# Kernel optimization log

Measured on AMD Instinct MI355X. Metric: run time of the kernel, lower is better.

The kernel has to match this reference:

```python
import jax, jax.numpy as jnp
import numpy as np

B, F, D = 1024, 64, 64  # batch, num fields, embedding dim


def setup_inputs() -> dict:
    key = jax.random.key(0)
    ks = jax.random.split(key, 7)
    return {
        "x": jax.random.normal(ks[0], (B, F, D), dtype=jnp.float32),
        "W1": jax.random.normal(ks[1], (F, F * F), dtype=jnp.float32) * 0.02,
        "b1": jax.random.normal(ks[2], (F,), dtype=jnp.float32) * 0.02,
        "W2": jax.random.normal(ks[3], (F, F * F), dtype=jnp.float32) * 0.02,
        "b2": jax.random.normal(ks[4], (F,), dtype=jnp.float32) * 0.02,
        "Wfc": jax.random.normal(ks[5], (1, 2 * F), dtype=jnp.float32) * 0.02,
        "bfc": jax.random.normal(ks[6], (1,), dtype=jnp.float32) * 0.02,
    }


def reference(x, W1, b1, W2, b2, Wfc, bfc):
    # x: [B, F, D]. CIN layer: outer product over field dims, 1x1 conv (channel
    # contraction with weight [F, F*F]), ReLU.
    b_, f0, d = x.shape
    x0 = x[:, :, None, :]  # [B, F, 1, D]
    h = x
    xs = []
    for W, b in ((W1, b1), (W2, b2)):
        z = (x0 * h[:, None, :, :]).reshape(b_, f0 * f0, d)  # [B, F*F, D]
        h = jax.nn.relu(jnp.einsum('oc,bcd->bod', W, z) + b[None, :, None])  # [B, F, D]
        xs.append(h)
    pooled = jnp.sum(jnp.concatenate(xs, axis=1), axis=2)  # [B, 2F] sum-pool over D
    return pooled @ Wfc.T + bfc  # [B, 1]
```

## Files before the change

### kernel.cpp

```cpp
#include <hip/hip_runtime.h>

typedef short s16x4 __attribute__((ext_vector_type(4)));
typedef short s16x8 __attribute__((ext_vector_type(8)));
typedef float f32x2 __attribute__((ext_vector_type(2)));
typedef float f32x16 __attribute__((ext_vector_type(16)));
typedef unsigned int u32x2 __attribute__((ext_vector_type(2)));
typedef unsigned int u32x4 __attribute__((ext_vector_type(4)));

#define HT_STRIDE 72

__device__ __forceinline__ unsigned short f2bf(float f) {
    unsigned int u = __float_as_uint(f);
    u += 0x7fffu + ((u >> 16) & 1u);
    return (unsigned short)(u >> 16);
}
__device__ __forceinline__ unsigned int pk2bf_rne(float lo, float hi) {
    unsigned int a = __float_as_uint(lo);
    a += 0x7fffu + ((a >> 16) & 1u);
    unsigned int b = __float_as_uint(hi);
    b += 0x7fffu + ((b >> 16) & 1u);
    return (a >> 16) | (b & 0xffff0000u);
}

__global__ __launch_bounds__(256) void prepack_kernel(const float* __restrict__ W1,
                                                      const float* __restrict__ W2,
                                                      unsigned short* __restrict__ Wp) {
    int tid = blockIdx.x * 256 + threadIdx.x;
    int lane = tid & 63;
    int ks = (tid >> 6) & 3;
    int jt = (tid >> 8) & 1;
    int o = (tid >> 9) & 63;
    int l = tid >> 15;
    int q2 = lane >> 5;
    int n31 = lane & 31;
    const float* W = l ? W2 : W1;
    const float* base = W + o * 4096 + jt * 32 + n31;
    int i0 = 16 * ks + 8 * q2;
    float v[8];
#pragma unroll
    for (int t = 0; t < 8; ++t) v[t] = base[(i0 + t) * 64];
    u32x4 pv;
    pv[0] = pk2bf_rne(v[0], v[1]);
    pv[1] = pk2bf_rne(v[2], v[3]);
    pv[2] = pk2bf_rne(v[4], v[5]);
    pv[3] = pk2bf_rne(v[6], v[7]);
    ((u32x4*)Wp)[tid] = pv;
}

__global__ __launch_bounds__(256, 2) void cin_kernel(const float* __restrict__ x,
                                                     const unsigned short* __restrict__ Wp,
                                                     const float* __restrict__ b1,
                                                     const float* __restrict__ b2,
                                                     const float* __restrict__ Wfc,
                                                     const float* __restrict__ bfc,
                                                     float* __restrict__ out) {
    __shared__ __align__(16) unsigned short sH[2][64 * HT_STRIDE];
    __shared__ float sBias[128], sWfc[128], sRed[4];

    const int tid = threadIdx.x;
    const int w = tid >> 6;
    const int lane = tid & 63;
    const int q2 = lane >> 5;
    const int n31 = lane & 31;
    const int oh = w;
    const int bb = blockIdx.x;

    {
        const float4* xb4 = (const float4*)(x + bb * 4096);
#pragma unroll
        for (int rr = 0; rr < 4; ++rr) {
            int e4 = rr * 256 + tid;
            float4 v = xb4[e4];
            int e = e4 << 2;
            int f = e >> 6;
            int d0 = e & 63;
            sH[0][(d0 + 0) * HT_STRIDE + f] = f2bf(v.x);
            sH[0][(d0 + 1) * HT_STRIDE + f] = f2bf(v.y);
            sH[0][(d0 + 2) * HT_STRIDE + f] = f2bf(v.z);
            sH[0][(d0 + 3) * HT_STRIDE + f] = f2bf(v.w);
        }
    }
    if (tid < 128) {
        sBias[tid] = (tid < 64) ? b1[tid] : b2[tid - 64];
        sWfc[tid] = Wfc[tid];
    }
    __syncthreads();

    const f32x16 zz = {};
    float contrib = 0.0f;
    const s16x8* WpS8 = (const s16x8*)Wp;

    s16x8 bfr[2][4];
#pragma unroll
    for (int nt = 0; nt < 2; ++nt) {
        const int d = nt * 32 + n31;
#pragma unroll
        for (int ks = 0; ks < 4; ++ks)
            bfr[nt][ks] = *(const s16x8*)&sH[0][d * HT_STRIDE + 16 * ks + 8 * q2];
    }

#define CONSUME(NT, ACC, JT, O)                                                   \
    {                                                                             \
        const f32x2* a2 = (const f32x2*)&(ACC);                                   \
        f32x2 s0 = {0.0f, 0.0f}, s1 = {0.0f, 0.0f};                               \
        _Pragma("unroll") for (int m = 0; m < 4; ++m) {                           \
            unsigned int qlo = cwp[NT][JT][m][0];                                 \
            unsigned int qhi = cwp[NT][JT][m][1];                                 \
            f32x2 c0 = {__uint_as_float(qlo << 16),                               \
                        __uint_as_float(qlo & 0xffff0000u)};                      \
            f32x2 c1 = {__uint_as_float(qhi << 16),                               \
                        __uint_as_float(qhi & 0xffff0000u)};                      \
            s0 += a2[2 * m] * c0;                                                 \
            s1 += a2[2 * m + 1] * c1;                                             \
        }                                                                         \
        f32x2 s = s0 + s1;                                                        \
        if ((JT) == 0) {                                                          \
            hp[NT] = s;                                                           \
        } else {                                                                  \
            f32x2 t2 = hp[NT] + s;                                                \
            float hsum = t2.x + t2.y;                                             \
            hsum += __shfl_xor(hsum, 32, 64);           \
            float v = fmaxf(hsum + sBias[l * 64 + (O)], 0.0f);                    \
            contrib += v * sWfc[l * 64 + (O)];                                    \
            if (l == 0)     \
                sH[1][((NT) * 32 + n31) * HT_STRIDE + (O)] = f2bf(v);             \
        }                                                                         \
    }

    for (int l = 0; l < 2; ++l) {
        if (l) __syncthreads();

        const unsigned short* hsrc = sH[l];
        u32x2 cwp[2][2][4];
#pragma unroll
        for (int nt = 0; nt < 2; ++nt) {
            const int d = nt * 32 + n31;
#pragma unroll
            for (int jt = 0; jt < 2; ++jt)
#pragma unroll
                for (int m = 0; m < 4; ++m)
                    cwp[nt][jt][m] =
                        *(const u32x2*)&hsrc[d * HT_STRIDE + jt * 32 + 4 * q2 + 8 * m];
        }

        s16x8 Areg[2][4];
        {
            const int F0 = (l * 128 + 2 * oh) * 4;
            const s16x8* p = WpS8 + F0 * 64 + lane;
#pragma unroll
            for (int ks = 0; ks < 4; ++ks) Areg[0][ks] = p[ks * 64];
        }
        f32x2 hp[2];

#pragma unroll 2
        for (int it = 0; it < 32; ++it) {
            const int jt = it & 1;
            const int o = 4 * (it >> 1) + oh;
            if (it < 31) {
                const int itn = it + 1;
                const int on = 4 * (itn >> 1) + oh;
                const int Fn = (l * 128 + 2 * on + (itn & 1)) * 4;
                const s16x8* p = WpS8 + Fn * 64 + lane;
#pragma unroll
                for (int ks = 0; ks < 4; ++ks) Areg[(it + 1) & 1][ks] = p[ks * 64];
            }
            const s16x8* A = Areg[it & 1];

            f32x16 a0 = __builtin_amdgcn_mfma_f32_32x32x16_bf16(A[0], bfr[0][0], zz, 0, 0, 0);
            a0 = __builtin_amdgcn_mfma_f32_32x32x16_bf16(A[1], bfr[0][1], a0, 0, 0, 0);
            a0 = __builtin_amdgcn_mfma_f32_32x32x16_bf16(A[2], bfr[0][2], a0, 0, 0, 0);
            a0 = __builtin_amdgcn_mfma_f32_32x32x16_bf16(A[3], bfr[0][3], a0, 0, 0, 0);
            CONSUME(0, a0, jt, o);
            __builtin_amdgcn_sched_barrier(0);

            f32x16 a1 = __builtin_amdgcn_mfma_f32_32x32x16_bf16(A[0], bfr[1][0], zz, 0, 0, 0);
            a1 = __builtin_amdgcn_mfma_f32_32x32x16_bf16(A[1], bfr[1][1], a1, 0, 0, 0);
            a1 = __builtin_amdgcn_mfma_f32_32x32x16_bf16(A[2], bfr[1][2], a1, 0, 0, 0);
            a1 = __builtin_amdgcn_mfma_f32_32x32x16_bf16(A[3], bfr[1][3], a1, 0, 0, 0);
            CONSUME(1, a1, jt, o);
        }
    }
#undef CONSUME

    contrib *= 0.5f;
#pragma unroll
    for (int off = 32; off > 0; off >>= 1)
        contrib += __shfl_down(contrib, off, 64);
    if (lane == 0) sRed[w] = contrib;
    __syncthreads();
    if (tid == 0)
        out[bb] = (sRed[0] + sRed[1]) + (sRed[2] + sRed[3]) + bfc[0];
}

extern "C" void kernel_launch(void* const* d_in, const int* in_sizes, int n_in,
                              void* d_out, int out_size, void* d_ws, size_t ws_size,
                              hipStream_t stream) {
    const float* x = (const float*)d_in[0];
    const float* W1 = (const float*)d_in[1];
    const float* b1 = (const float*)d_in[2];
    const float* W2 = (const float*)d_in[3];
    const float* b2 = (const float*)d_in[4];
    const float* Wfc = (const float*)d_in[5];
    const float* bfc = (const float*)d_in[6];
    float* out = (float*)d_out;

    unsigned short* Wp = (unsigned short*)d_ws;

    prepack_kernel<<<256, 256, 0, stream>>>(W1, W2, Wp);
    cin_kernel<<<1024, 256, 0, stream>>>(x, Wp, b1, b2, Wfc, bfc, out);
}
```

Baseline: 143.5 us.

## Deepen weight prefetch to a 4-stage inline-asm pipeline spanning both layers

Replaces the double-buffered weight-fragment loads with a 4-slot register ring filled by inline-asm global_load_dwordx4, issued three iterations ahead and continuing across the layer boundary. Explicit s_waitcnt vmcnt counts ensure only the current slot is complete before its MFMAs run. The two MFMA chains are also interleaved so both accumulators advance together instead of back to back. The aim is to hide global/L2 latency of the weight stream behind the matrix math, at the cost of more VGPRs, which could hurt occupancy with launch_bounds(256,2), and fragile hand-managed wait counts.

```diff
diff --git a/kernel.cpp b/kernel.cpp
--- a/kernel.cpp
+++ b/kernel.cpp
@@ -21,6 +21,10 @@
     b += 0x7fffu + ((b >> 16) & 1u);
     return (a >> 16) | (b & 0xffff0000u);
 }
+
+#define GLOADX4(dst, base, OFF)                                       \
+    asm volatile("global_load_dwordx4 %0, %1, off offset:" OFF        \
+                 : "=&v"(dst) : "v"(base) : "memory")
 
 __global__ __launch_bounds__(256) void prepack_kernel(const float* __restrict__ W1,
                                                       const float* __restrict__ W2,
@@ -64,6 +68,7 @@
     const int n31 = lane & 31;
     const int oh = w;
     const int bb = blockIdx.x;
+    const char* WpB = (const char*)Wp;
 
     {
         const float4* xb4 = (const float4*)(x + bb * 4096);
@@ -88,7 +93,19 @@
 
     const f32x16 zz = {};
     float contrib = 0.0f;
-    const s16x8* WpS8 = (const s16x8*)Wp;
+
+    s16x8 Ar[4][4];
+
+#pragma unroll
+    for (int g0 = 0; g0 < 3; ++g0) {
+        const int F = (8 * (g0 >> 1) + 2 * oh + (g0 & 1)) * 4;
+        const char* gp = WpB + (size_t)F * 1024 + lane * 16;
+        GLOADX4(Ar[g0][0], gp, "0");
+        GLOADX4(Ar[g0][1], gp, "1024");
+        GLOADX4(Ar[g0][2], gp, "2048");
+        GLOADX4(Ar[g0][3], gp, "3072");
+    }
+    __builtin_amdgcn_sched_barrier(0);
 
     s16x8 bfr[2][4];
 #pragma unroll
@@ -127,6 +144,44 @@
         }                                                                         \
     }
 
+#define ITER(IT, S)                                                               \
+    {                                                                             \
+        const int it_ = (IT);                                                     \
+        const int jt = it_ & 1;                                                   \
+        const int o = 4 * (it_ >> 1) + oh;                                        \
+        const int g = l * 32 + it_;                                               \
+        if (g < 61) {                                                             \
+            const int gn = g + 3;                                                 \
+            const int ln = gn >> 5, itn = gn & 31;                                \
+            const int Fn = (ln * 128 + 8 * (itn >> 1) + 2 * oh + (itn & 1)) * 4;  \
+            const char* gp = WpB + (size_t)Fn * 1024 + lane * 16;                 \
+            GLOADX4(Ar[((S) + 3) & 3][0], gp, "0");                               \
+            GLOADX4(Ar[((S) + 3) & 3][1], gp, "1024");                            \
+            GLOADX4(Ar[((S) + 3) & 3][2], gp, "2048");                            \
+            GLOADX4(Ar[((S) + 3) & 3][3], gp, "3072");                            \
+        }                                                                         \
+        __builtin_amdgcn_sched_barrier(0);                                        \
+        if (g < 61) {                                                             \
+            asm volatile("s_waitcnt vmcnt(12)" ::: "memory");                     \
+        } else if (g == 61) {                                                     \
+            asm volatile("s_waitcnt vmcnt(8)" ::: "memory");                      \
+        } else if (g == 62) {                                                     \
+            asm volatile("s_waitcnt vmcnt(4)" ::: "memory");                      \
+        } else {                                                                  \
+            asm volatile("s_waitcnt vmcnt(0)" ::: "memory");                      \
+        }                                                                         \
+        __builtin_amdgcn_sched_barrier(0);                                        \
+        const s16x8* A = Ar[(S)];                                                 \
+        f32x16 a0 = __builtin_amdgcn_mfma_f32_32x32x16_bf16(A[0], bfr[0][0], zz, 0, 0, 0); \
+        f32x16 a1 = __builtin_amdgcn_mfma_f32_32x32x16_bf16(A[0], bfr[1][0], zz, 0, 0, 0); \
+        _Pragma("unroll") for (int ks = 1; ks < 4; ++ks) {                        \
+            a0 = __builtin_amdgcn_mfma_f32_32x32x16_bf16(A[ks], bfr[0][ks], a0, 0, 0, 0); \
+            a1 = __builtin_amdgcn_mfma_f32_32x32x16_bf16(A[ks], bfr[1][ks], a1, 0, 0, 0); \
+        }                                                                         \
+        CONSUME(0, a0, jt, o);                                                    \
+        CONSUME(1, a1, jt, o);                                                    \
+    }
+
     for (int l = 0; l < 2; ++l) {
         if (l) __syncthreads();
 
@@ -143,43 +198,16 @@
                         *(const u32x2*)&hsrc[d * HT_STRIDE + jt * 32 + 4 * q2 + 8 * m];
         }
 
-        s16x8 Areg[2][4];
-        {
-            const int F0 = (l * 128 + 2 * oh) * 4;
-            const s16x8* p = WpS8 + F0 * 64 + lane;
-#pragma unroll
-            for (int ks = 0; ks < 4; ++ks) Areg[0][ks] = p[ks * 64];
+        f32x2 hp[2];
+
+        for (int itb = 0; itb < 32; itb += 4) {
+            ITER(itb + 0, 0);
+            ITER(itb + 1, 1);
+            ITER(itb + 2, 2);
+            ITER(itb + 3, 3);
         }
-        f32x2 hp[2];
-
-#pragma unroll 2
-        for (int it = 0; it < 32; ++it) {
-            const int jt = it & 1;
-            const int o = 4 * (it >> 1) + oh;
-            if (it < 31) {
-                const int itn = it + 1;
-                const int on = 4 * (itn >> 1) + oh;
-                const int Fn = (l * 128 + 2 * on + (itn & 1)) * 4;
-                const s16x8* p = WpS8 + Fn * 64 + lane;
-#pragma unroll
-                for (int ks = 0; ks < 4; ++ks) Areg[(it + 1) & 1][ks] = p[ks * 64];
-            }
-            const s16x8* A = Areg[it & 1];
-
-            f32x16 a0 = __builtin_amdgcn_mfma_f32_32x32x16_bf16(A[0], bfr[0][0], zz, 0, 0, 0);
-            a0 = __builtin_amdgcn_mfma_f32_32x32x16_bf16(A[1], bfr[0][1], a0, 0, 0, 0);
-            a0 = __builtin_amdgcn_mfma_f32_32x32x16_bf16(A[2], bfr[0][2], a0, 0, 0, 0);
-            a0 = __builtin_amdgcn_mfma_f32_32x32x16_bf16(A[3], bfr[0][3], a0, 0, 0, 0);
-            CONSUME(0, a0, jt, o);
-            __builtin_amdgcn_sched_barrier(0);
-
-            f32x16 a1 = __builtin_amdgcn_mfma_f32_32x32x16_bf16(A[0], bfr[1][0], zz, 0, 0, 0);
-            a1 = __builtin_amdgcn_mfma_f32_32x32x16_bf16(A[1], bfr[1][1], a1, 0, 0, 0);
-            a1 = __builtin_amdgcn_mfma_f32_32x32x16_bf16(A[2], bfr[1][2], a1, 0, 0, 0);
-            a1 = __builtin_amdgcn_mfma_f32_32x32x16_bf16(A[3], bfr[1][3], a1, 0, 0, 0);
-            CONSUME(1, a1, jt, o);
-        }
-    }
+    }
+#undef ITER
 #undef CONSUME
 
     contrib *= 0.5f;
```

Result: no change. 141.2 us (-1.6%).
